# Kernel tuning notes

Hardware: AMD Instinct MI355X
Metric: run time of the kernel (lower is better)

Reference implementation:

```python
import jax, jax.numpy as jnp
import numpy as np

N_NODES = 20000


def _gcn_norm(edge_index, n):
    src, dst = edge_index[0], edge_index[1]
    # degree of A + I (self-loops), all edge weights 1
    deg = jax.ops.segment_sum(jnp.ones(src.shape[0], jnp.float32), dst, num_segments=n) + 1.0
    dinv = jax.lax.rsqrt(deg)
    norm = dinv[src] * dinv[dst]          # [E]
    self_norm = dinv * dinv               # [N] self-loop coefficient = 1/deg
    return src, dst, norm, self_norm


def _gcn_layer(x, W, b, src, dst, norm, self_norm):
    # x: [B, N, Fin]; W: [Fin, Fout]
    h = jnp.einsum('bnf,fo->bno', x, W)   # transform first (PyG GCNConv order)
    msg = h[:, src, :] * norm[None, :, None]                      # [B, E, Fout]
    agg = jax.vmap(lambda m: jax.ops.segment_sum(m, dst, num_segments=x.shape[1]))(msg)
    agg = agg + h * self_norm[None, :, None]                      # self-loop term
    return agg + b


def setup_inputs() -> dict:
    key = jax.random.key(0)
    ks = jax.random.split(key, 8)
    B, N, Fin, H, O, E = 2, N_NODES, 256, 256, 64, 320000
    s = lambda f: 1.0 / np.sqrt(f)
    return {
        'x': jax.random.normal(ks[0], (B, N, Fin), jnp.float32),
        'W1': jax.random.normal(ks[1], (Fin, H), jnp.float32) * s(Fin),
        'b1': jnp.zeros((H,), jnp.float32),
        'W2': jax.random.normal(ks[2], (H, H), jnp.float32) * s(H),
        'b2': jnp.zeros((H,), jnp.float32),
        'Wfc': jax.random.normal(ks[3], (H, O), jnp.float32) * s(H),
        'bfc': jnp.zeros((O,), jnp.float32),
        'edge_index': jax.random.randint(ks[4], (2, E), 0, N, jnp.int64),
    }


def reference(x, W1, b1, W2, b2, Wfc, bfc, edge_index):
    src, dst, norm, self_norm = _gcn_norm(edge_index, x.shape[1])
    h = jax.nn.relu(_gcn_layer(x, W1, b1, src, dst, norm, self_norm))
    h = jax.nn.relu(_gcn_layer(h, W2, b2, src, dst, norm, self_norm))
    pooled = jnp.mean(h, axis=1)          # mean over nodes -> [B, H]
    return pooled @ Wfc + bfc             # [B, O]
```

## Files before the change

kernel.cpp:

```cpp
#include <hip/hip_runtime.h>

#define NNODES 20000
#define BATCH  2
#define FEAT   256
#define OOUT   64
#define PBLK   200
#define MROWS  40000
#define NPB    20096
#define H8ROWS 40192
#define NCHUNK 20

typedef short  bhalf8 __attribute__((ext_vector_type(8)));
typedef float  floatx4 __attribute__((ext_vector_type(4)));
typedef float  floatx2 __attribute__((ext_vector_type(2)));

__device__ __forceinline__ float bf2f(unsigned short u) {
  return __uint_as_float(((unsigned int)u) << 16);
}
__device__ __forceinline__ unsigned short f2bf(float f) {
  unsigned int u = __float_as_uint(f);
  return (unsigned short)((u + 0x7fffu + ((u >> 16) & 1u)) >> 16);
}
__device__ __forceinline__ unsigned int pack4_fp8(float a, float b, float c, float d) {
  int p = __builtin_amdgcn_cvt_pk_fp8_f32(a, b, 0, false);
  p = __builtin_amdgcn_cvt_pk_fp8_f32(c, d, p, true);
  return (unsigned int)p;
}

__global__ __launch_bounds__(256) void prep_kernel(const float* __restrict__ W1,
                                                   const float* __restrict__ W2,
                                                   unsigned short* __restrict__ w1hi,
                                                   unsigned short* __restrict__ w1lo,
                                                   unsigned short* __restrict__ w2hi,
                                                   unsigned short* __restrict__ w2lo,
                                                   const int* __restrict__ raw, int E,
                                                   int* __restrict__ flag,
                                                   int* __restrict__ cnt,
                                                   int* __restrict__ fill,
                                                   int* __restrict__ chunkOff) {
  int bid = blockIdx.x, tid = threadIdx.x;
  int idx = bid * 256 + tid;
  int which = idx >> 16, loc = idx & 65535;
  const float* W = which ? W2 : W1;
  unsigned short* Whi = which ? w2hi : w1hi;
  unsigned short* Wlo = which ? w2lo : w1lo;
  int k = loc >> 8, n = loc & 255;
  float w = W[loc];
  unsigned short hi = f2bf(w);
  unsigned short lo = f2bf(w - bf2f(hi));
  int g = n >> 4, ln = n & 15;
  int ks = k >> 5, ch = (k >> 3) & 3, j = k & 7;
  int addr = ((ks * 16 + g) * 64 + ch * 16 + ln) * 8 + j;
  Whi[addr] = hi;
  Wlo[addr] = lo;
  if (idx < NNODES) { cnt[idx] = 0; fill[idx] = 0; }
  if (idx < NCHUNK) chunkOff[idx] = 0;
  if (bid == 511) {
    __shared__ int any;
    if (tid == 0) any = 0;
    __syncthreads();
    int nchk = E < 2048 ? E : 2048;
    for (int i = tid; i < nchk; i += 256)
      if (raw[2 * i + 1] != 0) any = 1;
    __syncthreads();
    if (tid == 0) *flag = any;
  }
}

__global__ void count_kernel(const int* __restrict__ raw, const int* __restrict__ flag,
                             int* __restrict__ cnt, int E) {
  int e = blockIdx.x * blockDim.x + threadIdx.x;
  if (e >= E) return;
  int d = (*flag) ? raw[E + e] : raw[2 * (E + e)];
  atomicAdd(&cnt[d], 1);
}

__global__ __launch_bounds__(256) void scan_a_kernel(const int* __restrict__ cnt,
                                                     int* __restrict__ row_start,
                                                     float* __restrict__ dinv,
                                                     int* __restrict__ chunkOff) {
  int c = blockIdx.x, tid = threadIdx.x;
  int base = c * 1024 + tid * 4;
  int v[4]; int tsum = 0;
#pragma unroll
  for (int j = 0; j < 4; ++j) {
    v[j] = (base + j < NNODES) ? cnt[base + j] : 0;
    tsum += v[j];
  }
  int lane = tid & 63, wv = tid >> 6;
  int x = tsum;
#pragma unroll
  for (int off = 1; off < 64; off <<= 1) {
    int t = __shfl_up(x, off);
    if (lane >= off) x += t;
  }
  __shared__ int wsum[4];
  if (lane == 63) wsum[wv] = x;
  __syncthreads();
  int woff = 0;
  for (int w = 0; w < wv; ++w) woff += wsum[w];
  int run = woff + x - tsum;
#pragma unroll
  for (int j = 0; j < 4; ++j) {
    if (base + j <= NNODES) row_start[base + j] = run;
    if (base + j < NNODES) dinv[base + j] = 1.0f / sqrtf((float)(v[j] + 1));
    run += v[j];
  }
  if (tid == 0) {
    int T = wsum[0] + wsum[1] + wsum[2] + wsum[3];
    for (int c2 = c + 1; c2 < NCHUNK; ++c2) atomicAdd(&chunkOff[c2], T);
  }
}

__global__ void scatter_kernel(const int* __restrict__ raw, const int* __restrict__ flag,
                               const int* __restrict__ row_start, const int* __restrict__ chunkOff,
                               int* __restrict__ fill, const float* __restrict__ dinv,
                               int* __restrict__ csr_src, float* __restrict__ csr_norm, int E) {
  int e = blockIdx.x * blockDim.x + threadIdx.x;
  if (e >= E) return;
  int s, d;
  if (*flag) { s = raw[e];     d = raw[E + e]; }
  else       { s = raw[2 * e]; d = raw[2 * (E + e)]; }
  int p = row_start[d] + chunkOff[d >> 10] + atomicAdd(&fill[d], 1);
  csr_src[p] = s;
  csr_norm[p] = dinv[s] * dinv[d];
}

template <int AFP32>
__global__ __launch_bounds__(256) void gemm_mfma(const void* __restrict__ Av,
                                                 const unsigned short* __restrict__ Whi,
                                                 const unsigned short* __restrict__ Wlo,
                                                 unsigned int* __restrict__ C) {
  int bid = blockIdx.x;
  int tile = (bid >> 4) * 8 + (bid & 7);
  int half = (bid >> 3) & 1;
  if (tile >= 314) return;
  __shared__ unsigned short lds[2][8192];
  int b = tile >= 157 ? 1 : 0;
  int nbase = (tile - b * 157) * 128;
  int tid = threadIdx.x, lane = tid & 63, wv = tid >> 6;
  int kc = (lane >> 4) * 8;

  const float* Af          = (const float*)Av;
  const unsigned short* Ab = (const unsigned short*)Av;

  int nn[2], mr[2];
#pragma unroll
  for (int t = 0; t < 2; ++t) {
    int nl = nbase + wv * 32 + t * 16 + (lane & 15);
    nn[t] = nl;
    int ncl = nl > NNODES - 1 ? NNODES - 1 : nl;
    mr[t] = b * NNODES + ncl;
  }

  floatx4 acc[2][8];
#pragma unroll
  for (int t = 0; t < 2; ++t)
#pragma unroll
    for (int g = 0; g < 8; ++g) acc[t][g] = (floatx4)(0.0f);

  bhalf8 st[4];
  auto stage_load = [&](int ks) {
#pragma unroll
    for (int i2 = 0; i2 < 4; ++i2) {
      int u = i2 * 256 + tid;
      int hl = u >> 9, g = (u >> 6) & 7, l = u & 63;
      const unsigned short* Wp = hl ? Wlo : Whi;
      st[i2] = *(const bhalf8*)&Wp[((size_t)(ks * 16 + half * 8 + g) * 64 + l) * 8];
    }
  };
  auto stage_write = [&](int buf) {
#pragma unroll
    for (int i2 = 0; i2 < 4; ++i2) {
      int u = i2 * 256 + tid;
      *(bhalf8*)&lds[buf][(size_t)u * 8] = st[i2];
    }
  };
  auto load_a = [&](int ks, bhalf8 (&a)[2]) {
#pragma unroll
    for (int t = 0; t < 2; ++t) {
      if (AFP32) {
        const float* p = &Af[(size_t)mr[t] * FEAT + ks * 32 + kc];
        float4 u = *(const float4*)p;
        float4 v = *(const float4*)(p + 4);
        a[t][0] = (short)f2bf(u.x); a[t][1] = (short)f2bf(u.y);
        a[t][2] = (short)f2bf(u.z); a[t][3] = (short)f2bf(u.w);
        a[t][4] = (short)f2bf(v.x); a[t][5] = (short)f2bf(v.y);
        a[t][6] = (short)f2bf(v.z); a[t][7] = (short)f2bf(v.w);
      } else {
        a[t] = *(const bhalf8*)&Ab[(size_t)mr[t] * FEAT + ks * 32 + kc];
      }
    }
  };
  auto step = [&](int buf, bhalf8 (&a)[2]) {
#pragma unroll
    for (int g = 0; g < 8; ++g) {
      bhalf8 bh = *(const bhalf8*)&lds[buf][((size_t)g * 64 + lane) * 8];
      bhalf8 bl = *(const bhalf8*)&lds[buf][((size_t)(512 + g * 64) + lane) * 8];
#pragma unroll
      for (int t = 0; t < 2; ++t)
        acc[t][g] = __builtin_amdgcn_mfma_f32_16x16x32_bf16(bh, a[t], acc[t][g], 0, 0, 0);
#pragma unroll
      for (int t = 0; t < 2; ++t)
        acc[t][g] = __builtin_amdgcn_mfma_f32_16x16x32_bf16(bl, a[t], acc[t][g], 0, 0, 0);
    }
  };

  stage_load(0);
  stage_write(0);
  __syncthreads();
  bhalf8 aC[2];
  load_a(0, aC);
  int cur = 0;
#pragma unroll
  for (int ks = 0; ks < 8; ++ks) {
    bhalf8 aN[2];
    if (ks < 7) {
      stage_load(ks + 1);
      load_a(ks + 1, aN);
    }
    step(cur, aC);
    if (ks < 7) {
      stage_write(cur ^ 1);
      __syncthreads();
      aC[0] = aN[0]; aC[1] = aN[1];
    }
    cur ^= 1;
  }

  int nc = (lane >> 4) * 4;
#pragma unroll
  for (int t = 0; t < 2; ++t) {
    size_t r = (size_t)nn[t] * 2 + b;
#pragma unroll
    for (int g = 0; g < 8; ++g) {
      int col = (half * 8 + g) * 16 + nc;
      C[r * 64 + (col >> 2)] =
          pack4_fp8(acc[t][g][0], acc[t][g][1], acc[t][g][2], acc[t][g][3]);
    }
  }
}

__global__ __launch_bounds__(128) void agg_kernel(const uint4* __restrict__ h8,
                                                  const int* __restrict__ row_start,
                                                  const int* __restrict__ chunkOff,
                                                  const int* __restrict__ csr_src,
                                                  const float* __restrict__ csr_norm,
                                                  const float* __restrict__ dinv,
                                                  const float* __restrict__ bias,
                                                  unsigned short* __restrict__ out) {
  int n = blockIdx.x;
  int tid = threadIdx.x;
  int wave = tid >> 6, lane = tid & 63;
  int q = (wave << 1) | (lane >> 5);
  int cl = lane & 31;

  float a[16];
#pragma unroll
  for (int j = 0; j < 16; ++j) a[j] = 0.0f;

  auto dec_fma = [&](uint4 m, float w) {
    unsigned int mm[4] = {m.x, m.y, m.z, m.w};
#pragma unroll
    for (int j = 0; j < 4; ++j) {
      floatx2 lo = __builtin_amdgcn_cvt_pk_f32_fp8((int)mm[j], false);
      floatx2 hi = __builtin_amdgcn_cvt_pk_f32_fp8((int)mm[j], true);
      a[j * 4 + 0] = fmaf(w, lo[0], a[j * 4 + 0]);
      a[j * 4 + 1] = fmaf(w, lo[1], a[j * 4 + 1]);
      a[j * 4 + 2] = fmaf(w, hi[0], a[j * 4 + 2]);
      a[j * 4 + 3] = fmaf(w, hi[1], a[j * 4 + 3]);
    }
  };

  float di = dinv[n];
  if (q == 0) dec_fma(h8[(size_t)n * 32 + cl], di * di);

  int s0 = row_start[n] + chunkOff[n >> 10];
  int s1 = row_start[n + 1] + chunkOff[(n + 1) >> 10];
  int i = s0 + q;
  for (; i + 4 < s1; i += 8) {
    int sa = csr_src[i], sb = csr_src[i + 4];
    float wa = csr_norm[i], wb = csr_norm[i + 4];
    uint4 ma = h8[(size_t)sa * 32 + cl];
    uint4 mb = h8[(size_t)sb * 32 + cl];
    dec_fma(ma, wa);
    dec_fma(mb, wb);
  }
  if (i < s1) dec_fma(h8[(size_t)csr_src[i] * 32 + cl], csr_norm[i]);

#pragma unroll
  for (int j = 0; j < 16; ++j) a[j] += __shfl_xor(a[j], 32);

  __shared__ float red[32][17];
  if (wave == 1 && lane < 32) {
#pragma unroll
    for (int j = 0; j < 16; ++j) red[lane][j] = a[j];
  }
  __syncthreads();
  if (wave == 0 && lane < 32) {
    int b = cl >> 4;
    int c = (cl & 15) * 16;
#pragma unroll
    for (int j = 0; j < 16; ++j) a[j] += red[lane][j];
    unsigned short o[16];
#pragma unroll
    for (int j = 0; j < 16; ++j)
      o[j] = f2bf(fmaxf(a[j] + bias[c + j], 0.0f));
    unsigned short* dst = &out[((size_t)b * NNODES + n) * FEAT + c];
    *(uint4*)dst = *(uint4*)&o[0];
    *(uint4*)(dst + 8) = *(uint4*)&o[8];
  }
}

__global__ __launch_bounds__(256) void pool_partial(const unsigned short* __restrict__ h2,
                                                    float* __restrict__ partials) {
  int blk = blockIdx.x;
  int c = threadIdx.x;
  int chunk = NNODES / PBLK;
  int n0 = blk * chunk;
  float s0 = 0.f, s1 = 0.f;
  for (int n = n0; n < n0 + chunk; ++n) {
    s0 += bf2f(h2[((size_t)0 * NNODES + n) * FEAT + c]);
    s1 += bf2f(h2[((size_t)1 * NNODES + n) * FEAT + c]);
  }
  partials[(blk * 2 + 0) * FEAT + c] = s0;
  partials[(blk * 2 + 1) * FEAT + c] = s1;
}

__global__ __launch_bounds__(256) void pool_fc(const float* __restrict__ partials,
                                               const float* __restrict__ Wfc, const float* __restrict__ bfc,
                                               float* __restrict__ out) {
  __shared__ float pooled[BATCH][FEAT];
  int t = threadIdx.x;
  float s0 = 0.f, s1 = 0.f;
  for (int p = 0; p < PBLK; ++p) {
    s0 += partials[(p * 2 + 0) * FEAT + t];
    s1 += partials[(p * 2 + 1) * FEAT + t];
  }
  pooled[0][t] = s0 / (float)NNODES;
  pooled[1][t] = s1 / (float)NNODES;
  __syncthreads();
  if (t < BATCH * OOUT) {
    int b = t >> 6, o = t & 63;
    float acc = bfc[o];
    for (int c2 = 0; c2 < FEAT; ++c2)
      acc = fmaf(pooled[b][c2], Wfc[c2 * OOUT + o], acc);
    out[b * OOUT + o] = acc;
  }
}

extern "C" void kernel_launch(void* const* d_in, const int* in_sizes, int n_in,
                              void* d_out, int out_size, void* d_ws, size_t ws_size,
                              hipStream_t stream) {
  const float* x    = (const float*)d_in[0];
  const float* W1   = (const float*)d_in[1];
  const float* b1   = (const float*)d_in[2];
  const float* W2   = (const float*)d_in[3];
  const float* b2   = (const float*)d_in[4];
  const float* Wfc  = (const float*)d_in[5];
  const float* bfc  = (const float*)d_in[6];
  const int*   eraw = (const int*)d_in[7];
  int E = in_sizes[7] / 2;
  float* out = (float*)d_out;

  char* ws = (char*)d_ws;
  size_t off = 0;
  auto alloc = [&](size_t elems4B) -> void* {
    void* p = ws + off * 4;
    off += (elems4B + 3) & ~(size_t)3;
    return p;
  };
  int*   flag      = (int*)alloc(4);
  int*   cnt       = (int*)alloc(NNODES);
  float* dinv      = (float*)alloc(NNODES);
  int*   row_start = (int*)alloc(NNODES + 1);
  int*   fill      = (int*)alloc(NNODES);
  int*   chunkOff  = (int*)alloc(NCHUNK + 4);
  int*   csr_src   = (int*)alloc(E);
  float* csr_norm  = (float*)alloc(E);
  unsigned short* w1hi = (unsigned short*)alloc(65536 / 2);
  unsigned short* w1lo = (unsigned short*)alloc(65536 / 2);
  unsigned short* w2hi = (unsigned short*)alloc(65536 / 2);
  unsigned short* w2lo = (unsigned short*)alloc(65536 / 2);
  unsigned int*   h8   = (unsigned int*)alloc((size_t)H8ROWS * 64);
  unsigned short* a1   = (unsigned short*)alloc((size_t)MROWS * FEAT / 2);
  float* partials  = (float*)alloc((size_t)PBLK * BATCH * FEAT);

  int eg = (E + 255) / 256;
  prep_kernel<<<512, 256, 0, stream>>>(W1, W2, w1hi, w1lo, w2hi, w2lo, eraw, E, flag,
                                       cnt, fill, chunkOff);
  count_kernel<<<eg, 256, 0, stream>>>(eraw, flag, cnt, E);
  scan_a_kernel<<<NCHUNK, 256, 0, stream>>>(cnt, row_start, dinv, chunkOff);
  scatter_kernel<<<eg, 256, 0, stream>>>(eraw, flag, row_start, chunkOff, fill, dinv,
                                         csr_src, csr_norm, E);

  gemm_mfma<1><<<640, 256, 0, stream>>>(x, w1hi, w1lo, h8);
  agg_kernel<<<NNODES, 128, 0, stream>>>((const uint4*)h8, row_start, chunkOff,
                                         csr_src, csr_norm, dinv, b1, a1);
  gemm_mfma<0><<<640, 256, 0, stream>>>(a1, w2hi, w2lo, h8);
  agg_kernel<<<NNODES, 128, 0, stream>>>((const uint4*)h8, row_start, chunkOff,
                                         csr_src, csr_norm, dinv, b2, a1);
  pool_partial<<<PBLK, 256, 0, stream>>>(a1, partials);
  pool_fc<<<1, 256, 0, stream>>>(partials, Wfc, bfc, out);
}
```

Baseline: 177.9 us.

## Fold edge counting into first GEMM, fuse pooling with FC, deepen gather unroll

Degree counting now runs in extra blocks appended to the first GEMM launch, and that GEMM launch moves ahead of the CSR build. The two pooling kernels become one, with a last-block ticket (atomic counter plus threadfences) doing the final reduction and FC. The aggregation loop now keeps four gathers in flight per iteration instead of two. This removes two kernel launches and raises memory-level parallelism in the gather, at the cost of more registers and atomic/fence ordering complexity.

Result: slower. 190.3 us (+7.0%).

```diff
diff --git a/kernel.cpp b/kernel.cpp
--- a/kernel.cpp
+++ b/kernel.cpp
@@ -9,6 +9,7 @@
 #define NPB    20096
 #define H8ROWS 40192
 #define NCHUNK 20
+#define GEMMB  640
 
 typedef short  bhalf8 __attribute__((ext_vector_type(8)));
 typedef float  floatx4 __attribute__((ext_vector_type(4)));
@@ -37,7 +38,8 @@
                                                    int* __restrict__ flag,
                                                    int* __restrict__ cnt,
                                                    int* __restrict__ fill,
-                                                   int* __restrict__ chunkOff) {
+                                                   int* __restrict__ chunkOff,
+                                                   int* __restrict__ poolCnt) {
   int bid = blockIdx.x, tid = threadIdx.x;
   int idx = bid * 256 + tid;
   int which = idx >> 16, loc = idx & 65535;
@@ -55,6 +57,7 @@
   Wlo[addr] = lo;
   if (idx < NNODES) { cnt[idx] = 0; fill[idx] = 0; }
   if (idx < NCHUNK) chunkOff[idx] = 0;
+  if (idx == 0) *poolCnt = 0;
   if (bid == 511) {
     __shared__ int any;
     if (tid == 0) any = 0;
@@ -65,14 +68,6 @@
     __syncthreads();
     if (tid == 0) *flag = any;
   }
-}
-
-__global__ void count_kernel(const int* __restrict__ raw, const int* __restrict__ flag,
-                             int* __restrict__ cnt, int E) {
-  int e = blockIdx.x * blockDim.x + threadIdx.x;
-  if (e >= E) return;
-  int d = (*flag) ? raw[E + e] : raw[2 * (E + e)];
-  atomicAdd(&cnt[d], 1);
 }
 
 __global__ __launch_bounds__(256) void scan_a_kernel(const int* __restrict__ cnt,
@@ -126,19 +121,32 @@
   csr_norm[p] = dinv[s] * dinv[d];
 }
 
-template <int AFP32>
+template <int AFP32, int CNT>
 __global__ __launch_bounds__(256) void gemm_mfma(const void* __restrict__ Av,
                                                  const unsigned short* __restrict__ Whi,
                                                  const unsigned short* __restrict__ Wlo,
-                                                 unsigned int* __restrict__ C) {
+                                                 unsigned int* __restrict__ C,
+                                                 const int* __restrict__ raw,
+                                                 const int* __restrict__ flag,
+                                                 int* __restrict__ cnt, int E) {
   int bid = blockIdx.x;
+  int tid = threadIdx.x, lane = tid & 63, wv = tid >> 6;
+  if (bid >= GEMMB) {
+    if (CNT) {
+      int e = (bid - GEMMB) * 256 + tid;
+      if (e < E) {
+        int d = (*flag) ? raw[E + e] : raw[2 * (E + e)];
+        atomicAdd(&cnt[d], 1);
+      }
+    }
+    return;
+  }
   int tile = (bid >> 4) * 8 + (bid & 7);
   int half = (bid >> 3) & 1;
   if (tile >= 314) return;
   __shared__ unsigned short lds[2][8192];
   int b = tile >= 157 ? 1 : 0;
   int nbase = (tile - b * 157) * 128;
-  int tid = threadIdx.x, lane = tid & 63, wv = tid >> 6;
   int kc = (lane >> 4) * 8;
 
   const float* Af          = (const float*)Av;
@@ -278,15 +286,19 @@
   int s0 = row_start[n] + chunkOff[n >> 10];
   int s1 = row_start[n + 1] + chunkOff[(n + 1) >> 10];
   int i = s0 + q;
-  for (; i + 4 < s1; i += 8) {
-    int sa = csr_src[i], sb = csr_src[i + 4];
-    float wa = csr_norm[i], wb = csr_norm[i + 4];
-    uint4 ma = h8[(size_t)sa * 32 + cl];
-    uint4 mb = h8[(size_t)sb * 32 + cl];
-    dec_fma(ma, wa);
-    dec_fma(mb, wb);
-  }
-  if (i < s1) dec_fma(h8[(size_t)csr_src[i] * 32 + cl], csr_norm[i]);
+  for (; i + 12 < s1; i += 16) {
+    int   sa[4];
+    float wa[4];
+    uint4 m[4];
+#pragma unroll
+    for (int j = 0; j < 4; ++j) { sa[j] = csr_src[i + 4 * j]; wa[j] = csr_norm[i + 4 * j]; }
+#pragma unroll
+    for (int j = 0; j < 4; ++j) m[j] = h8[(size_t)sa[j] * 32 + cl];
+#pragma unroll
+    for (int j = 0; j < 4; ++j) dec_fma(m[j], wa[j]);
+  }
+  for (; i < s1; i += 4)
+    dec_fma(h8[(size_t)csr_src[i] * 32 + cl], csr_norm[i]);
 
 #pragma unroll
   for (int j = 0; j < 16; ++j) a[j] += __shfl_xor(a[j], 32);
@@ -312,8 +324,12 @@
   }
 }
 
-__global__ __launch_bounds__(256) void pool_partial(const unsigned short* __restrict__ h2,
-                                                    float* __restrict__ partials) {
+__global__ __launch_bounds__(256) void pool_kernel(const unsigned short* __restrict__ h2,
+                                                   const float* __restrict__ Wfc,
+                                                   const float* __restrict__ bfc,
+                                                   float* __restrict__ partials,
+                                                   int* __restrict__ poolCnt,
+                                                   float* __restrict__ out) {
   int blk = blockIdx.x;
   int c = threadIdx.x;
   int chunk = NNODES / PBLK;
@@ -325,23 +341,24 @@
   }
   partials[(blk * 2 + 0) * FEAT + c] = s0;
   partials[(blk * 2 + 1) * FEAT + c] = s1;
-}
-
-__global__ __launch_bounds__(256) void pool_fc(const float* __restrict__ partials,
-                                               const float* __restrict__ Wfc, const float* __restrict__ bfc,
-                                               float* __restrict__ out) {
+  __threadfence();
+  __shared__ int ticket;
+  if (c == 0) ticket = atomicAdd(poolCnt, 1);
+  __syncthreads();
+  if (ticket != PBLK - 1) return;
+  __threadfence();
+
   __shared__ float pooled[BATCH][FEAT];
-  int t = threadIdx.x;
-  float s0 = 0.f, s1 = 0.f;
+  float t0 = 0.f, t1 = 0.f;
   for (int p = 0; p < PBLK; ++p) {
-    s0 += partials[(p * 2 + 0) * FEAT + t];
-    s1 += partials[(p * 2 + 1) * FEAT + t];
-  }
-  pooled[0][t] = s0 / (float)NNODES;
-  pooled[1][t] = s1 / (float)NNODES;
+    t0 += partials[(p * 2 + 0) * FEAT + c];
+    t1 += partials[(p * 2 + 1) * FEAT + c];
+  }
+  pooled[0][c] = t0 / (float)NNODES;
+  pooled[1][c] = t1 / (float)NNODES;
   __syncthreads();
-  if (t < BATCH * OOUT) {
-    int b = t >> 6, o = t & 63;
+  if (c < BATCH * OOUT) {
+    int b = c >> 6, o = c & 63;
     float acc = bfc[o];
     for (int c2 = 0; c2 < FEAT; ++c2)
       acc = fmaf(pooled[b][c2], Wfc[c2 * OOUT + o], acc);
@@ -376,6 +393,7 @@
   int*   row_start = (int*)alloc(NNODES + 1);
   int*   fill      = (int*)alloc(NNODES);
   int*   chunkOff  = (int*)alloc(NCHUNK + 4);
+  int*   poolCnt   = (int*)alloc(4);
   int*   csr_src   = (int*)alloc(E);
   float* csr_norm  = (float*)alloc(E);
   unsigned short* w1hi = (unsigned short*)alloc(65536 / 2);
@@ -388,18 +406,15 @@
 
   int eg = (E + 255) / 256;
   prep_kernel<<<512, 256, 0, stream>>>(W1, W2, w1hi, w1lo, w2hi, w2lo, eraw, E, flag,
-                                       cnt, fill, chunkOff);
-  count_kernel<<<eg, 256, 0, stream>>>(eraw, flag, cnt, E);
+                                       cnt, fill, chunkOff, poolCnt);
+  gemm_mfma<1, 1><<<GEMMB + eg, 256, 0, stream>>>(x, w1hi, w1lo, h8, eraw, flag, cnt, E);
   scan_a_kernel<<<NCHUNK, 256, 0, stream>>>(cnt, row_start, dinv, chunkOff);
   scatter_kernel<<<eg, 256, 0, stream>>>(eraw, flag, row_start, chunkOff, fill, dinv,
                                          csr_src, csr_norm, E);
-
-  gemm_mfma<1><<<640, 256, 0, stream>>>(x, w1hi, w1lo, h8);
   agg_kernel<<<NNODES, 128, 0, stream>>>((const uint4*)h8, row_start, chunkOff,
                                          csr_src, csr_norm, dinv, b1, a1);
-  gemm_mfma<0><<<640, 256, 0, stream>>>(a1, w2hi, w2lo, h8);
+  gemm_mfma<0, 0><<<GEMMB, 256, 0, stream>>>(a1, w2hi, w2lo, h8, nullptr, nullptr, nullptr, 0);
   agg_kernel<<<NNODES, 128, 0, stream>>>((const uint4*)h8, row_start, chunkOff,
                                          csr_src, csr_norm, dinv, b2, a1);
-  pool_partial<<<PBLK, 256, 0, stream>>>(a1, partials);
-  pool_fc<<<1, 256, 0, stream>>>(partials, Wfc, bfc, out);
-}
+  pool_kernel<<<PBLK, 256, 0, stream>>>(a1, Wfc, bfc, partials, poolCnt, out);
+}
```
